# Performance work log

Hardware: AMD Instinct MI355X
Metric: run time of the kernel (lower is better)

## Reference

```python
import jax, jax.numpy as jnp
import numpy as np

N, E, D = 50000, 800000, 128
CLAMP = 2.0  # coord_weights_clamp_value


def setup_inputs() -> dict:
    key = jax.random.key(0)
    ks = jax.random.split(key, 12)
    rn = lambda k, shape, scale: jax.random.normal(k, shape, jnp.float32) * scale
    s = lambda fan_in: 1.0 / np.sqrt(fan_in)
    h = rn(ks[0], (N, D), 1.0)
    x = rn(ks[1], (N, 3), 1.0)
    edges = jax.random.randint(ks[2], (2, E), 0, N)
    # edge MLP: Linear(2D+1 -> D), SiLU, Linear(D -> D), SiLU
    we1 = rn(ks[3], (2 * D + 1, D), s(2 * D + 1)); be1 = jnp.zeros((D,), jnp.float32)
    we2 = rn(ks[4], (D, D), s(D));                 be2 = jnp.zeros((D,), jnp.float32)
    # node MLP: Linear(2D -> D), SiLU, Linear(D -> D)
    wn1 = rn(ks[5], (2 * D, D), s(2 * D));         bn1 = jnp.zeros((D,), jnp.float32)
    wn2 = rn(ks[6], (D, D), s(D));                 bn2 = jnp.zeros((D,), jnp.float32)
    # coord MLP: Linear(D -> D), SiLU, Linear(D -> 1, no bias, small init)
    wc1 = rn(ks[7], (D, D), s(D));                 bc1 = jnp.zeros((D,), jnp.float32)
    wc2 = rn(ks[8], (D, 1), 0.001)
    return dict(h=h, x=x, edges=edges, we1=we1, be1=be1, we2=we2, be2=be2,
                wn1=wn1, bn1=bn1, wn2=wn2, bn2=bn2, wc1=wc1, bc1=bc1, wc2=wc2)


def reference(h, x, edges, we1, be1, we2, be2, wn1, bn1, wn2, bn2, wc1, bc1, wc2):
    n = h.shape[0]
    row, col = edges[0], edges[1]
    # coord2radial
    coord_diff = x[row] - x[col]                                  # [E, 3]
    radial = jnp.sum(coord_diff * coord_diff, axis=1, keepdims=True)  # [E, 1]
    # edge model: phi_e(h_i, h_j, ||x_i - x_j||^2)
    e_in = jnp.concatenate([h[row], h[col], radial], axis=1)      # [E, 2D+1]
    m = jax.nn.silu(jax.nn.silu(e_in @ we1 + be1) @ we2 + be2)    # [E, D]
    # coord model: x_i += mean_j (x_i - x_j) * phi_x(m_ij), clamped
    w = jax.nn.silu(m @ wc1 + bc1) @ wc2                          # [E, 1]
    trans = jnp.clip(coord_diff * w, -CLAMP, CLAMP)               # [E, 3]
    ones = jnp.ones((row.shape[0], 1), m.dtype)
    cnt = jax.ops.segment_sum(ones, row, num_segments=n)          # [N, 1]
    agg_x = jax.ops.segment_sum(trans, row, num_segments=n) / jnp.maximum(cnt, 1.0)
    x_out = x + agg_x
    # node model: h_i += phi_h(h_i, sum_j m_ij)  (residual=True)
    agg_m = jax.ops.segment_sum(m, row, num_segments=n)           # [N, D]
    h_up = jax.nn.silu(jnp.concatenate([h, agg_m], axis=1) @ wn1 + bn1) @ wn2 + bn2
    h_out = h + h_up
    return (h_out, x_out)
```

## Files before the change

### kernel.cpp

```cpp
#include <hip/hip_runtime.h>
#include <hip/hip_bf16.h>
#include <stdint.h>

typedef unsigned short u16;
typedef __bf16 bf16x8 __attribute__((ext_vector_type(8)));
typedef float f32x4 __attribute__((ext_vector_type(4)));
typedef unsigned int u32x4 __attribute__((ext_vector_type(4)));

#define DD 128

__device__ __forceinline__ u16 f2bf(float f) {
  uint32_t r;
  asm("v_cvt_pk_bf16_f32 %0, %1, %2" : "=v"(r) : "v"(f), "v"(f));
  return (u16)r;
}
__device__ __forceinline__ float bf2f(u16 h) {
  union { uint32_t u; float f; } v; v.u = ((uint32_t)h) << 16;
  return v.f;
}
__device__ __forceinline__ uint32_t pack2(float a, float b) {
  uint32_t r;
  asm("v_cvt_pk_bf16_f32 %0, %1, %2" : "=v"(r) : "v"(a), "v"(b));
  return r;
}
__device__ __forceinline__ float silu_(float v) {
  return v * __builtin_amdgcn_rcpf(1.0f + __expf(-v));
}
__device__ __forceinline__ f32x4 MFMA(bf16x8 a, bf16x8 b, f32x4 c) {
  return __builtin_amdgcn_mfma_f32_16x16x32_bf16(a, b, c, 0, 0, 0);
}
#define LGKM_FENCE() do { asm volatile("s_waitcnt lgkmcnt(0)" ::: "memory"); __builtin_amdgcn_sched_barrier(0); } while (0)

__global__ __launch_bounds__(256) void kprep(
    const float* __restrict__ we1, const float* __restrict__ we2,
    const float* __restrict__ wn1, const float* __restrict__ wn2,
    const float* __restrict__ wc1, u16* __restrict__ frags) {
  const int total = 16384 * 5 + 32768;
  for (int idx = blockIdx.x * blockDim.x + threadIdx.x; idx < total;
       idx += gridDim.x * blockDim.x) {
    const float* src; int segbase;
    if (idx < 16384)      { src = we1;          segbase = 0; }
    else if (idx < 32768) { src = we1 + 16384;  segbase = 16384; }
    else if (idx < 49152) { src = we2;          segbase = 32768; }
    else if (idx < 65536) { src = wc1;          segbase = 49152; }
    else if (idx < 81920) { src = wn2;          segbase = 65536; }
    else                  { src = wn1;          segbase = 81920; }
    int local = idx - segbase;
    int k = local >> 7, n = local & 127;
    float v = src[k * 128 + n];
    int s = k >> 5, i = k & 7, g = (k >> 3) & 3;
    int lane = (g << 4) | (n & 15), f = n >> 4;
    frags[segbase + (((s * 8 + f) * 64 + lane) << 3) + i] = f2bf(v);
  }
}

__global__ __launch_bounds__(256) void kradial(
    const int* __restrict__ edges, const float* __restrict__ x,
    uint2* __restrict__ cdr, int E) {
  int i = blockIdx.x * 256 + threadIdx.x;
  if (i >= E) return;
  int r = edges[i], c = edges[E + i];
  float dx = x[r * 3]     - x[c * 3];
  float dy = x[r * 3 + 1] - x[c * 3 + 1];
  float dz = x[r * 3 + 2] - x[c * 3 + 2];
  float rad = dx * dx + dy * dy + dz * dz;
  cdr[i] = make_uint2(pack2(dx, dy), pack2(dz, rad));
}

__global__ __launch_bounds__(256) void kpq(
    const float* __restrict__ h, const float* __restrict__ be1,
    const u16* __restrict__ wA, const u16* __restrict__ wB,
    u16* __restrict__ Pb, u16* __restrict__ Qb, int N) {
  __shared__ u16 act[64 * 128];
  const int tid = threadIdx.x;
  const int w = tid >> 6, l = tid & 63;
  const int lm = l & 15, lh = l >> 4;
  const int base = blockIdx.x * 64;

  {
    const int q = l & 3;
    const int rowL = w * 16 + (l >> 2);
    int node = base + rowL; if (node >= N) node = N - 1;
    const float* hs = h + (size_t)node * 128 + q * 32;
    #pragma unroll
    for (int c4 = 0; c4 < 4; ++c4) {
      float4 v0 = *(const float4*)(hs + c4 * 8);
      float4 v1 = *(const float4*)(hs + c4 * 8 + 4);
      uint4 pk;
      pk.x = pack2(v0.x, v0.y); pk.y = pack2(v0.z, v0.w);
      pk.z = pack2(v1.x, v1.y); pk.w = pack2(v1.z, v1.w);
      int c = q * 4 + c4;
      *(uint4*)&act[rowL * 128 + (((c ^ (rowL & 7))) << 3)] = pk;
    }
  }
  LGKM_FENCE();
  const int rowA = w * 16 + lm, sw = rowA & 7;
  bf16x8 a[4];
  #pragma unroll
  for (int s = 0; s < 4; ++s)
    a[s] = *(const bf16x8*)&act[rowA * 128 + (((4 * s + lh) ^ sw) << 3)];
  float be1r[8];
  #pragma unroll
  for (int f = 0; f < 8; ++f) be1r[f] = be1[16 * f + lm];

  f32x4 acc[8] = {};
  #pragma unroll
  for (int s = 0; s < 4; ++s)
    #pragma unroll
    for (int f = 0; f < 8; ++f)
      acc[f] = MFMA(a[s], *(const bf16x8*)(wA + (((s * 8 + f) * 64 + l) << 3)), acc[f]);
  #pragma unroll
  for (int f = 0; f < 8; ++f)
    #pragma unroll
    for (int r = 0; r < 4; ++r) {
      int row = base + w * 16 + lh * 4 + r;
      Pb[(size_t)row * 128 + 16 * f + lm] = f2bf(acc[f][r] + be1r[f]);
    }

  f32x4 acc2[8] = {};
  #pragma unroll
  for (int s = 0; s < 4; ++s)
    #pragma unroll
    for (int f = 0; f < 8; ++f)
      acc2[f] = MFMA(a[s], *(const bf16x8*)(wB + (((s * 8 + f) * 64 + l) << 3)), acc2[f]);
  #pragma unroll
  for (int f = 0; f < 8; ++f)
    #pragma unroll
    for (int r = 0; r < 4; ++r) {
      int row = base + w * 16 + lh * 4 + r;
      Qb[(size_t)row * 128 + 16 * f + lm] = f2bf(acc2[f][r]);
    }
}

__global__ __launch_bounds__(256) void kedgeP(
    const int* __restrict__ edges, const uint2* __restrict__ cdr,
    const float* __restrict__ we1, const float* __restrict__ be2,
    const float* __restrict__ bc1, const float* __restrict__ wc2,
    const u16* __restrict__ Pb, const u16* __restrict__ Qb,
    const u16* __restrict__ we2f, const u16* __restrict__ wc1f,
    float* __restrict__ aggm, float* __restrict__ aggx, int E) {
  __shared__ u16 act[64 * 128];
  __shared__ float w1c[128];
  const int tid = threadIdx.x;
  if (tid < 128) w1c[tid] = we1[256 * 128 + tid];
  __syncthreads();

  const int w = tid >> 6, l = tid & 63;
  const int lm = l & 15, lh = l >> 4;
  const int el = l >> 2, q = l & 3;
  float be2r[8], bc1r[8], wc2r[8];
  #pragma unroll
  for (int f = 0; f < 8; ++f) {
    be2r[f] = be2[16 * f + lm];
    bc1r[f] = bc1[16 * f + lm];
    wc2r[f] = wc2[16 * f + lm];
  }

  const int tb = blockIdx.x * 256 + w * 64;
  const int rowA = w * 16 + lm, sw = rowA & 7;
  const int rowL = w * 16 + el;

  int rv[4], cv[4]; uint2 cdu[4];
  #pragma unroll
  for (int t = 0; t < 4; ++t) {
    int e = tb + t * 16 + lm;
    int ec = e < E ? e : E - 1;
    rv[t] = edges[ec];
    cv[t] = edges[E + ec];
    cdu[t] = cdr[ec];
  }

  u32x4 Pc[4], Qc[4], Pn[4], Qn[4];
  {
    int rG = __shfl(rv[0], el), cG = __shfl(cv[0], el);
    const u16* Pp = Pb + (size_t)rG * 128 + q * 32;
    const u16* Qp = Qb + (size_t)cG * 128 + q * 32;
    #pragma unroll
    for (int c4 = 0; c4 < 4; ++c4) {
      Pc[c4] = *(const u32x4*)(Pp + c4 * 8);
      Qc[c4] = *(const u32x4*)(Qp + c4 * 8);
    }
  }

  #pragma unroll
  for (int t = 0; t < 4; ++t) {
    {
      float radf = bf2f((u16)(cdu[t].y >> 16));
      float rad = __shfl(radf, el);
      #pragma unroll
      for (int c4 = 0; c4 < 4; ++c4) {
        uint32_t pw[4] = {Pc[c4].x, Pc[c4].y, Pc[c4].z, Pc[c4].w};
        uint32_t qw[4] = {Qc[c4].x, Qc[c4].y, Qc[c4].z, Qc[c4].w};
        uint32_t ow[4];
        #pragma unroll
        for (int jj = 0; jj < 4; ++jj) {
          int fb = q * 32 + c4 * 8 + jj * 2;
          float t0 = bf2f((u16)(pw[jj] & 0xffff)) + bf2f((u16)(qw[jj] & 0xffff)) + rad * w1c[fb];
          float t1 = bf2f((u16)(pw[jj] >> 16))    + bf2f((u16)(qw[jj] >> 16))    + rad * w1c[fb + 1];
          ow[jj] = pack2(silu_(t0), silu_(t1));
        }
        int c = q * 4 + c4;
        *(uint4*)&act[rowL * 128 + ((c ^ (rowL & 7)) << 3)] =
            make_uint4(ow[0], ow[1], ow[2], ow[3]);
      }
    }
    LGKM_FENCE();

    bf16x8 a[4];
    #pragma unroll
    for (int s = 0; s < 4; ++s)
      a[s] = *(const bf16x8*)&act[rowA * 128 + (((4 * s + lh) ^ sw) << 3)];

    if (t < 3) {
      int rG = __shfl(rv[t + 1], el), cG = __shfl(cv[t + 1], el);
      const u16* Pp = Pb + (size_t)rG * 128 + q * 32;
      const u16* Qp = Qb + (size_t)cG * 128 + q * 32;
      #pragma unroll
      for (int c4 = 0; c4 < 4; ++c4) {
        Pn[c4] = *(const u32x4*)(Pp + c4 * 8);
        Qn[c4] = *(const u32x4*)(Qp + c4 * 8);
      }
    }

    f32x4 acc[8] = {};
    #pragma unroll
    for (int s = 0; s < 4; ++s)
      #pragma unroll
      for (int f = 0; f < 8; ++f)
        acc[f] = MFMA(a[s], *(const bf16x8*)(we2f + (((s * 8 + f) * 64 + l) << 3)), acc[f]);

    uint32_t pk_m[8][2];
    #pragma unroll
    for (int f = 0; f < 8; ++f) {
      float mv[4];
      #pragma unroll
      for (int r = 0; r < 4; ++r) {
        mv[r] = silu_(acc[f][r] + be2r[f]);
        int row = w * 16 + lh * 4 + r, col = 16 * f + lm;
        act[row * 128 + (((col >> 3) ^ (row & 7)) << 3) + (col & 7)] = f2bf(mv[r]);
      }
      pk_m[f][0] = pack2(mv[0], mv[1]);
      pk_m[f][1] = pack2(mv[2], mv[3]);
    }
    LGKM_FENCE();

    bf16x8 a2[4];
    #pragma unroll
    for (int s = 0; s < 4; ++s)
      a2[s] = *(const bf16x8*)&act[rowA * 128 + (((4 * s + lh) ^ sw) << 3)];
    f32x4 acc3[8] = {};
    #pragma unroll
    for (int s = 0; s < 4; ++s)
      #pragma unroll
      for (int f = 0; f < 8; ++f)
        acc3[f] = MFMA(a2[s], *(const bf16x8*)(wc1f + (((s * 8 + f) * 64 + l) << 3)), acc3[f]);

    float wp[4] = {0.f, 0.f, 0.f, 0.f};
    #pragma unroll
    for (int f = 0; f < 8; ++f)
      #pragma unroll
      for (int r = 0; r < 4; ++r)
        wp[r] += silu_(acc3[f][r] + bc1r[f]) * wc2r[f];
    #pragma unroll
    for (int r = 0; r < 4; ++r) {
      wp[r] += __shfl_xor(wp[r], 1);
      wp[r] += __shfl_xor(wp[r], 2);
      wp[r] += __shfl_xor(wp[r], 4);
      wp[r] += __shfl_xor(wp[r], 8);
    }

    float cdx = bf2f((u16)(cdu[t].x & 0xffff));
    float cdy = bf2f((u16)(cdu[t].x >> 16));
    float cdz = bf2f((u16)(cdu[t].y & 0xffff));
    int er[4]; bool vr[4];
    float cdxr[4], cdyr[4], cdzr[4];
    #pragma unroll
    for (int r = 0; r < 4; ++r) {
      er[r] = __shfl(rv[t], lh * 4 + r);
      vr[r] = (tb + t * 16 + lh * 4 + r) < E;
      cdxr[r] = __shfl(cdx, lh * 4 + r);
      cdyr[r] = __shfl(cdy, lh * 4 + r);
      cdzr[r] = __shfl(cdz, lh * 4 + r);
    }

    if (lm < 4) {
      #pragma unroll
      for (int r = 0; r < 4; ++r) {
        if (vr[r]) {
          float wv = wp[r];
          float v3;
          if (lm == 0)      v3 = fminf(fmaxf(cdxr[r] * wv, -2.0f), 2.0f);
          else if (lm == 1) v3 = fminf(fmaxf(cdyr[r] * wv, -2.0f), 2.0f);
          else if (lm == 2) v3 = fminf(fmaxf(cdzr[r] * wv, -2.0f), 2.0f);
          else              v3 = 1.0f;
          unsafeAtomicAdd(&aggx[(size_t)er[r] * 4 + lm], v3);
        }
      }
    }

    #pragma unroll
    for (int f = 0; f < 8; ++f)
      #pragma unroll
      for (int r = 0; r < 4; ++r) {
        if (vr[r]) {
          float m = bf2f((u16)((pk_m[f][r >> 1] >> ((r & 1) * 16)) & 0xffff));
          unsafeAtomicAdd(&aggm[(size_t)er[r] * 128 + 16 * f + lm], m);
        }
      }

    if (t < 3) {
      #pragma unroll
      for (int c4 = 0; c4 < 4; ++c4) { Pc[c4] = Pn[c4]; Qc[c4] = Qn[c4]; }
    }
  }
}

__global__ __launch_bounds__(256) void kedge_mono(
    const float* __restrict__ x, const int* __restrict__ edges,
    const float* __restrict__ we1, const float* __restrict__ be2,
    const float* __restrict__ bc1, const float* __restrict__ wc2,
    const u16* __restrict__ Pb, const u16* __restrict__ Qb,
    const u16* __restrict__ we2f, const u16* __restrict__ wc1f,
    float* __restrict__ aggm, float* __restrict__ aggx, int E) {
  __shared__ u16 act[64 * 128];
  __shared__ float w1c[128];
  const int tid = threadIdx.x;
  if (tid < 128) w1c[tid] = we1[256 * 128 + tid];
  __syncthreads();

  const int w = tid >> 6, l = tid & 63;
  const int lm = l & 15, lh = l >> 4;
  float be2r[8], bc1r[8], wc2r[8];
  #pragma unroll
  for (int f = 0; f < 8; ++f) {
    be2r[f] = be2[16 * f + lm];
    bc1r[f] = bc1[16 * f + lm];
    wc2r[f] = wc2[16 * f + lm];
  }

  const int tb = blockIdx.x * 64 + w * 16;
  int eMine = tb + lm;
  int eC = eMine < E ? eMine : E - 1;
  const int rowv = edges[eC];
  const int colv = edges[E + eC];
  float cdx = x[rowv * 3]     - x[colv * 3];
  float cdy = x[rowv * 3 + 1] - x[colv * 3 + 1];
  float cdz = x[rowv * 3 + 2] - x[colv * 3 + 2];
  float radial = cdx * cdx + cdy * cdy + cdz * cdz;

  {
    const int el = l >> 2, q = l & 3;
    int rG = __shfl(rowv, el), cG = __shfl(colv, el);
    float rad = __shfl(radial, el);
    const int rowL = w * 16 + el;
    const u16* Pp = Pb + (size_t)rG * 128 + q * 32;
    const u16* Qp = Qb + (size_t)cG * 128 + q * 32;
    #pragma unroll
    for (int c4 = 0; c4 < 4; ++c4) {
      uint4 pv = *(const uint4*)(Pp + c4 * 8);
      uint4 qv = *(const uint4*)(Qp + c4 * 8);
      uint32_t pw[4] = {pv.x, pv.y, pv.z, pv.w};
      uint32_t qw[4] = {qv.x, qv.y, qv.z, qv.w};
      uint32_t ow[4];
      #pragma unroll
      for (int t2 = 0; t2 < 4; ++t2) {
        int fb = q * 32 + c4 * 8 + t2 * 2;
        float t0 = bf2f((u16)(pw[t2] & 0xffff)) + bf2f((u16)(qw[t2] & 0xffff)) + rad * w1c[fb];
        float t1 = bf2f((u16)(pw[t2] >> 16))    + bf2f((u16)(qw[t2] >> 16))    + rad * w1c[fb + 1];
        ow[t2] = pack2(silu_(t0), silu_(t1));
      }
      int c = q * 4 + c4;
      *(uint4*)&act[rowL * 128 + ((c ^ (rowL & 7)) << 3)] =
          make_uint4(ow[0], ow[1], ow[2], ow[3]);
    }
  }
  LGKM_FENCE();

  const int rowA = w * 16 + lm, sw = rowA & 7;
  bf16x8 a[4];
  #pragma unroll
  for (int s = 0; s < 4; ++s)
    a[s] = *(const bf16x8*)&act[rowA * 128 + (((4 * s + lh) ^ sw) << 3)];

  f32x4 acc[8] = {};
  #pragma unroll
  for (int s = 0; s < 4; ++s)
    #pragma unroll
    for (int f = 0; f < 8; ++f)
      acc[f] = MFMA(a[s], *(const bf16x8*)(we2f + (((s * 8 + f) * 64 + l) << 3)), acc[f]);

  #pragma unroll
  for (int f = 0; f < 8; ++f)
    #pragma unroll
    for (int r = 0; r < 4; ++r) {
      float m = silu_(acc[f][r] + be2r[f]);
      int row = w * 16 + lh * 4 + r, col = 16 * f + lm;
      act[row * 128 + (((col >> 3) ^ (row & 7)) << 3) + (col & 7)] = f2bf(m);
    }
  LGKM_FENCE();

  bf16x8 a2[4];
  #pragma unroll
  for (int s = 0; s < 4; ++s)
    a2[s] = *(const bf16x8*)&act[rowA * 128 + (((4 * s + lh) ^ sw) << 3)];
  f32x4 acc3[8] = {};
  #pragma unroll
  for (int s = 0; s < 4; ++s)
    #pragma unroll
    for (int f = 0; f < 8; ++f)
      acc3[f] = MFMA(a2[s], *(const bf16x8*)(wc1f + (((s * 8 + f) * 64 + l) << 3)), acc3[f]);

  float wp[4] = {0.f, 0.f, 0.f, 0.f};
  #pragma unroll
  for (int f = 0; f < 8; ++f)
    #pragma unroll
    for (int r = 0; r < 4; ++r)
      wp[r] += silu_(acc3[f][r] + bc1r[f]) * wc2r[f];
  #pragma unroll
  for (int r = 0; r < 4; ++r) {
    wp[r] += __shfl_xor(wp[r], 1);
    wp[r] += __shfl_xor(wp[r], 2);
    wp[r] += __shfl_xor(wp[r], 4);
    wp[r] += __shfl_xor(wp[r], 8);
  }
  int er[4]; bool vr[4];
  float cdxr[4], cdyr[4], cdzr[4];
  #pragma unroll
  for (int r = 0; r < 4; ++r) {
    er[r] = __shfl(rowv, lh * 4 + r);
    vr[r] = (tb + lh * 4 + r) < E;
    cdxr[r] = __shfl(cdx, lh * 4 + r);
    cdyr[r] = __shfl(cdy, lh * 4 + r);
    cdzr[r] = __shfl(cdz, lh * 4 + r);
  }

  if (lm < 4) {
    #pragma unroll
    for (int r = 0; r < 4; ++r) {
      if (vr[r]) {
        float wv = wp[r];
        float v3;
        if (lm == 0)      v3 = fminf(fmaxf(cdxr[r] * wv, -2.0f), 2.0f);
        else if (lm == 1) v3 = fminf(fmaxf(cdyr[r] * wv, -2.0f), 2.0f);
        else if (lm == 2) v3 = fminf(fmaxf(cdzr[r] * wv, -2.0f), 2.0f);
        else              v3 = 1.0f;
        unsafeAtomicAdd(&aggx[(size_t)er[r] * 4 + lm], v3);
      }
    }
  }
  #pragma unroll
  for (int f = 0; f < 8; ++f)
    #pragma unroll
    for (int r = 0; r < 4; ++r) {
      if (vr[r]) {
        float m = silu_(acc[f][r] + be2r[f]);
        unsafeAtomicAdd(&aggm[(size_t)er[r] * 128 + 16 * f + lm], m);
      }
    }
}

__global__ __launch_bounds__(256) void knode(
    const float* __restrict__ h, const float* __restrict__ x,
    const float* __restrict__ aggm, const float* __restrict__ aggx,
    const float* __restrict__ bn1, const float* __restrict__ bn2,
    const u16* __restrict__ wn1f, const u16* __restrict__ wn2f,
    float* __restrict__ out, int N) {
  __shared__ u16 act[64 * 256];
  __shared__ u16 act2[64 * 128];
  const int tid = threadIdx.x;
  const int w = tid >> 6, l = tid & 63;
  const int lm = l & 15, lh = l >> 4;
  const int base = blockIdx.x * 64;

  if (tid < 192) {
    int n = base + tid / 3, c = tid - (tid / 3) * 3;
    if (n < N) {
      float ct = fmaxf(aggx[(size_t)n * 4 + 3], 1.0f);
      out[(size_t)N * 128 + (size_t)n * 3 + c] =
          x[(size_t)n * 3 + c] + aggx[(size_t)n * 4 + c] / ct;
    }
  }

  {
    const int q = l & 3;
    const int rowL = w * 16 + (l >> 2);
    int node = base + rowL; if (node >= N) node = N - 1;
    const float* src = (q < 2) ? (h + (size_t)node * 128 + q * 64)
                               : (aggm + (size_t)node * 128 + (q - 2) * 64);
    #pragma unroll
    for (int c8 = 0; c8 < 8; ++c8) {
      float4 v0 = *(const float4*)(src + c8 * 8);
      float4 v1 = *(const float4*)(src + c8 * 8 + 4);
      uint4 pk;
      pk.x = pack2(v0.x, v0.y); pk.y = pack2(v0.z, v0.w);
      pk.z = pack2(v1.x, v1.y); pk.w = pack2(v1.z, v1.w);
      int c = q * 8 + c8;
      *(uint4*)&act[rowL * 256 + ((c ^ (rowL & 7)) << 3)] = pk;
    }
  }
  LGKM_FENCE();

  const int rowA = w * 16 + lm, sw = rowA & 7;
  float bn1r[8], bn2r[8];
  #pragma unroll
  for (int f = 0; f < 8; ++f) {
    bn1r[f] = bn1[16 * f + lm];
    bn2r[f] = bn2[16 * f + lm];
  }
  bf16x8 a[8];
  #pragma unroll
  for (int s = 0; s < 8; ++s)
    a[s] = *(const bf16x8*)&act[rowA * 256 + (((4 * s + lh) ^ sw) << 3)];
  f32x4 acc[8] = {};
  #pragma unroll
  for (int s = 0; s < 8; ++s)
    #pragma unroll
    for (int f = 0; f < 8; ++f)
      acc[f] = MFMA(a[s], *(const bf16x8*)(wn1f + (((s * 8 + f) * 64 + l) << 3)), acc[f]);
  #pragma unroll
  for (int f = 0; f < 8; ++f)
    #pragma unroll
    for (int r = 0; r < 4; ++r) {
      int row = w * 16 + lh * 4 + r, col = 16 * f + lm;
      act2[row * 128 + (((col >> 3) ^ (row & 7)) << 3) + (col & 7)] =
          f2bf(silu_(acc[f][r] + bn1r[f]));
    }
  LGKM_FENCE();

  bf16x8 a2[4];
  #pragma unroll
  for (int s = 0; s < 4; ++s)
    a2[s] = *(const bf16x8*)&act2[rowA * 128 + (((4 * s + lh) ^ sw) << 3)];
  f32x4 acc2[8] = {};
  #pragma unroll
  for (int s = 0; s < 4; ++s)
    #pragma unroll
    for (int f = 0; f < 8; ++f)
      acc2[f] = MFMA(a2[s], *(const bf16x8*)(wn2f + (((s * 8 + f) * 64 + l) << 3)), acc2[f]);
  #pragma unroll
  for (int f = 0; f < 8; ++f)
    #pragma unroll
    for (int r = 0; r < 4; ++r) {
      int n2 = base + w * 16 + lh * 4 + r;
      if (n2 < N) {
        int col = 16 * f + lm;
        out[(size_t)n2 * 128 + col] =
            h[(size_t)n2 * 128 + col] + acc2[f][r] + bn2r[f];
      }
    }
}

extern "C" void kernel_launch(void* const* d_in, const int* in_sizes, int n_in,
                              void* d_out, int out_size, void* d_ws, size_t ws_size,
                              hipStream_t stream) {
  const float* h   = (const float*)d_in[0];
  const float* x   = (const float*)d_in[1];
  const int* edges = (const int*)d_in[2];
  const float* we1 = (const float*)d_in[3];
  const float* be1 = (const float*)d_in[4];
  const float* we2 = (const float*)d_in[5];
  const float* be2 = (const float*)d_in[6];
  const float* wn1 = (const float*)d_in[7];
  const float* bn1 = (const float*)d_in[8];
  const float* wn2 = (const float*)d_in[9];
  const float* bn2 = (const float*)d_in[10];
  const float* wc1 = (const float*)d_in[11];
  const float* bc1 = (const float*)d_in[12];
  const float* wc2 = (const float*)d_in[13];

  const int N = in_sizes[0] / DD;
  const int E = in_sizes[2] / 2;
  const int NT = (N + 63) & ~63;

  u16* Pb    = (u16*)d_ws;
  u16* Qb    = Pb + (size_t)NT * DD;
  u16* frags = Qb + (size_t)NT * DD;
  float* aggm = (float*)(frags + 114688);
  float* aggx = aggm + (size_t)NT * DD;
  uint2* cdr = (uint2*)(aggx + (size_t)NT * 4);

  size_t need_mono = (size_t)NT * DD * 2 * 2 + 114688 * 2 +
                     (size_t)NT * (DD * 4 + 16);
  size_t need_pipe = need_mono + (size_t)E * 8;
  if (ws_size < need_mono) return;

  hipLaunchKernelGGL(kprep, dim3(64), dim3(256), 0, stream,
                     we1, we2, wn1, wn2, wc1, frags);
  hipLaunchKernelGGL(kpq, dim3(NT / 64), dim3(256), 0, stream,
                     h, be1, frags, frags + 16384, Pb, Qb, N);
  hipMemsetAsync(aggm, 0, (size_t)NT * (DD * 4 + 16), stream);

  if (ws_size >= need_pipe) {
    hipLaunchKernelGGL(kradial, dim3((E + 255) / 256), dim3(256), 0, stream,
                       edges, x, cdr, E);
    hipLaunchKernelGGL(kedgeP, dim3((E + 255) / 256), dim3(256), 0, stream,
                       edges, cdr, we1, be2, bc1, wc2, Pb, Qb,
                       frags + 32768, frags + 49152, aggm, aggx, E);
  } else {
    hipLaunchKernelGGL(kedge_mono, dim3((E + 63) / 64), dim3(256), 0, stream,
                       x, edges, we1, be2, bc1, wc2, Pb, Qb,
                       frags + 32768, frags + 49152, aggm, aggx, E);
  }
  hipLaunchKernelGGL(knode, dim3(NT / 64), dim3(256), 0, stream,
                     h, x, aggm, aggx, bn1, bn2,
                     frags + 81920, frags + 65536, (float*)d_out, N);
}
```

Before: 551.1 us.

## Replace pipelined 4-tile edge kernel with one-tile-per-wave slim kernel

The edge kernel now has each wave process a single 16-edge tile instead of looping over four tiles with software-prefetched P/Q gathers. The grid is four times larger. MFMA accumulators are split into two halves of four, and bias loads are done inline instead of kept in registers, all to cut register pressure and raise occupancy. The coordinate atomics are also spread across all 64 lanes rather than 4 lanes per row. The trade-off is losing the explicit gather/compute overlap and re-running the per-block w1c shared-memory setup more often.

```diff
diff --git a/kernel.cpp b/kernel.cpp
--- a/kernel.cpp
+++ b/kernel.cpp
@@ -132,12 +132,13 @@
     }
 }
 
-__global__ __launch_bounds__(256) void kedgeP(
+__global__ __launch_bounds__(256) void kedge_slim(
     const int* __restrict__ edges, const uint2* __restrict__ cdr,
-    const float* __restrict__ we1, const float* __restrict__ be2,
-    const float* __restrict__ bc1, const float* __restrict__ wc2,
+    const float* __restrict__ be2, const float* __restrict__ bc1,
+    const float* __restrict__ wc2,
     const u16* __restrict__ Pb, const u16* __restrict__ Qb,
     const u16* __restrict__ we2f, const u16* __restrict__ wc1f,
+    const float* __restrict__ we1,
     float* __restrict__ aggm, float* __restrict__ aggx, int E) {
   __shared__ u16 act[64 * 128];
   __shared__ float w1c[128];
@@ -148,171 +149,139 @@
   const int w = tid >> 6, l = tid & 63;
   const int lm = l & 15, lh = l >> 4;
   const int el = l >> 2, q = l & 3;
-  float be2r[8], bc1r[8], wc2r[8];
-  #pragma unroll
-  for (int f = 0; f < 8; ++f) {
-    be2r[f] = be2[16 * f + lm];
-    bc1r[f] = bc1[16 * f + lm];
-    wc2r[f] = wc2[16 * f + lm];
-  }
-
-  const int tb = blockIdx.x * 256 + w * 64;
-  const int rowA = w * 16 + lm, sw = rowA & 7;
-  const int rowL = w * 16 + el;
-
-  int rv[4], cv[4]; uint2 cdu[4];
-  #pragma unroll
-  for (int t = 0; t < 4; ++t) {
-    int e = tb + t * 16 + lm;
-    int ec = e < E ? e : E - 1;
-    rv[t] = edges[ec];
-    cv[t] = edges[E + ec];
-    cdu[t] = cdr[ec];
-  }
-
-  u32x4 Pc[4], Qc[4], Pn[4], Qn[4];
+
+  const int tb = blockIdx.x * 64 + w * 16;
+  int eMine = tb + lm;
+  int eC = eMine < E ? eMine : E - 1;
+  const int rowv = edges[eC];
+  const int colv = edges[E + eC];
+  const uint2 cdu = cdr[eC];
+
   {
-    int rG = __shfl(rv[0], el), cG = __shfl(cv[0], el);
+    int rG = __shfl(rowv, el), cG = __shfl(colv, el);
+    float radf = bf2f((u16)(cdu.y >> 16));
+    float rad = __shfl(radf, el);
+    const int rowL = w * 16 + el;
     const u16* Pp = Pb + (size_t)rG * 128 + q * 32;
     const u16* Qp = Qb + (size_t)cG * 128 + q * 32;
     #pragma unroll
     for (int c4 = 0; c4 < 4; ++c4) {
-      Pc[c4] = *(const u32x4*)(Pp + c4 * 8);
-      Qc[c4] = *(const u32x4*)(Qp + c4 * 8);
-    }
-  }
-
-  #pragma unroll
-  for (int t = 0; t < 4; ++t) {
-    {
-      float radf = bf2f((u16)(cdu[t].y >> 16));
-      float rad = __shfl(radf, el);
+      u32x4 pv = *(const u32x4*)(Pp + c4 * 8);
+      u32x4 qv = *(const u32x4*)(Qp + c4 * 8);
+      uint32_t pw[4] = {pv.x, pv.y, pv.z, pv.w};
+      uint32_t qw[4] = {qv.x, qv.y, qv.z, qv.w};
+      uint32_t ow[4];
       #pragma unroll
-      for (int c4 = 0; c4 < 4; ++c4) {
-        uint32_t pw[4] = {Pc[c4].x, Pc[c4].y, Pc[c4].z, Pc[c4].w};
-        uint32_t qw[4] = {Qc[c4].x, Qc[c4].y, Qc[c4].z, Qc[c4].w};
-        uint32_t ow[4];
-        #pragma unroll
-        for (int jj = 0; jj < 4; ++jj) {
-          int fb = q * 32 + c4 * 8 + jj * 2;
-          float t0 = bf2f((u16)(pw[jj] & 0xffff)) + bf2f((u16)(qw[jj] & 0xffff)) + rad * w1c[fb];
-          float t1 = bf2f((u16)(pw[jj] >> 16))    + bf2f((u16)(qw[jj] >> 16))    + rad * w1c[fb + 1];
-          ow[jj] = pack2(silu_(t0), silu_(t1));
-        }
-        int c = q * 4 + c4;
-        *(uint4*)&act[rowL * 128 + ((c ^ (rowL & 7)) << 3)] =
-            make_uint4(ow[0], ow[1], ow[2], ow[3]);
-      }
-    }
-    LGKM_FENCE();
-
-    bf16x8 a[4];
-    #pragma unroll
-    for (int s = 0; s < 4; ++s)
-      a[s] = *(const bf16x8*)&act[rowA * 128 + (((4 * s + lh) ^ sw) << 3)];
-
-    if (t < 3) {
-      int rG = __shfl(rv[t + 1], el), cG = __shfl(cv[t + 1], el);
-      const u16* Pp = Pb + (size_t)rG * 128 + q * 32;
-      const u16* Qp = Qb + (size_t)cG * 128 + q * 32;
-      #pragma unroll
-      for (int c4 = 0; c4 < 4; ++c4) {
-        Pn[c4] = *(const u32x4*)(Pp + c4 * 8);
-        Qn[c4] = *(const u32x4*)(Qp + c4 * 8);
-      }
-    }
-
-    f32x4 acc[8] = {};
+      for (int jj = 0; jj < 4; ++jj) {
+        int fb = q * 32 + c4 * 8 + jj * 2;
+        float t0 = bf2f((u16)(pw[jj] & 0xffff)) + bf2f((u16)(qw[jj] & 0xffff)) + rad * w1c[fb];
+        float t1 = bf2f((u16)(pw[jj] >> 16))    + bf2f((u16)(qw[jj] >> 16))    + rad * w1c[fb + 1];
+        ow[jj] = pack2(silu_(t0), silu_(t1));
+      }
+      int c = q * 4 + c4;
+      *(uint4*)&act[rowL * 128 + ((c ^ (rowL & 7)) << 3)] =
+          make_uint4(ow[0], ow[1], ow[2], ow[3]);
+    }
+  }
+  LGKM_FENCE();
+
+  const int rowA = w * 16 + lm, sw = rowA & 7;
+  bf16x8 a[4];
+  #pragma unroll
+  for (int s = 0; s < 4; ++s)
+    a[s] = *(const bf16x8*)&act[rowA * 128 + (((4 * s + lh) ^ sw) << 3)];
+
+  uint32_t pk_m[8][2];
+  #pragma unroll
+  for (int half = 0; half < 2; ++half) {
+    f32x4 acc[4] = {};
     #pragma unroll
     for (int s = 0; s < 4; ++s)
       #pragma unroll
-      for (int f = 0; f < 8; ++f)
-        acc[f] = MFMA(a[s], *(const bf16x8*)(we2f + (((s * 8 + f) * 64 + l) << 3)), acc[f]);
-
-    uint32_t pk_m[8][2];
-    #pragma unroll
-    for (int f = 0; f < 8; ++f) {
+      for (int f = 0; f < 4; ++f)
+        acc[f] = MFMA(a[s],
+            *(const bf16x8*)(we2f + (((s * 8 + half * 4 + f) * 64 + l) << 3)),
+            acc[f]);
+    #pragma unroll
+    for (int f = 0; f < 4; ++f) {
+      const int F = half * 4 + f;
+      float be2v = be2[16 * F + lm];
       float mv[4];
       #pragma unroll
       for (int r = 0; r < 4; ++r) {
-        mv[r] = silu_(acc[f][r] + be2r[f]);
-        int row = w * 16 + lh * 4 + r, col = 16 * f + lm;
+        mv[r] = silu_(acc[f][r] + be2v);
+        int row = w * 16 + lh * 4 + r, col = 16 * F + lm;
         act[row * 128 + (((col >> 3) ^ (row & 7)) << 3) + (col & 7)] = f2bf(mv[r]);
       }
-      pk_m[f][0] = pack2(mv[0], mv[1]);
-      pk_m[f][1] = pack2(mv[2], mv[3]);
-    }
-    LGKM_FENCE();
-
-    bf16x8 a2[4];
-    #pragma unroll
-    for (int s = 0; s < 4; ++s)
-      a2[s] = *(const bf16x8*)&act[rowA * 128 + (((4 * s + lh) ^ sw) << 3)];
-    f32x4 acc3[8] = {};
+      pk_m[F][0] = pack2(mv[0], mv[1]);
+      pk_m[F][1] = pack2(mv[2], mv[3]);
+    }
+  }
+  LGKM_FENCE();
+
+  bf16x8 a2[4];
+  #pragma unroll
+  for (int s = 0; s < 4; ++s)
+    a2[s] = *(const bf16x8*)&act[rowA * 128 + (((4 * s + lh) ^ sw) << 3)];
+  float wp[4] = {0.f, 0.f, 0.f, 0.f};
+  #pragma unroll
+  for (int half = 0; half < 2; ++half) {
+    f32x4 acc3[4] = {};
     #pragma unroll
     for (int s = 0; s < 4; ++s)
       #pragma unroll
-      for (int f = 0; f < 8; ++f)
-        acc3[f] = MFMA(a2[s], *(const bf16x8*)(wc1f + (((s * 8 + f) * 64 + l) << 3)), acc3[f]);
-
-    float wp[4] = {0.f, 0.f, 0.f, 0.f};
-    #pragma unroll
-    for (int f = 0; f < 8; ++f)
+      for (int f = 0; f < 4; ++f)
+        acc3[f] = MFMA(a2[s],
+            *(const bf16x8*)(wc1f + (((s * 8 + half * 4 + f) * 64 + l) << 3)),
+            acc3[f]);
+    #pragma unroll
+    for (int f = 0; f < 4; ++f) {
+      const int F = half * 4 + f;
+      float bc1v = bc1[16 * F + lm];
+      float wc2v = wc2[16 * F + lm];
       #pragma unroll
       for (int r = 0; r < 4; ++r)
-        wp[r] += silu_(acc3[f][r] + bc1r[f]) * wc2r[f];
-    #pragma unroll
-    for (int r = 0; r < 4; ++r) {
-      wp[r] += __shfl_xor(wp[r], 1);
-      wp[r] += __shfl_xor(wp[r], 2);
-      wp[r] += __shfl_xor(wp[r], 4);
-      wp[r] += __shfl_xor(wp[r], 8);
-    }
-
-    float cdx = bf2f((u16)(cdu[t].x & 0xffff));
-    float cdy = bf2f((u16)(cdu[t].x >> 16));
-    float cdz = bf2f((u16)(cdu[t].y & 0xffff));
-    int er[4]; bool vr[4];
-    float cdxr[4], cdyr[4], cdzr[4];
-    #pragma unroll
-    for (int r = 0; r < 4; ++r) {
-      er[r] = __shfl(rv[t], lh * 4 + r);
-      vr[r] = (tb + t * 16 + lh * 4 + r) < E;
-      cdxr[r] = __shfl(cdx, lh * 4 + r);
-      cdyr[r] = __shfl(cdy, lh * 4 + r);
-      cdzr[r] = __shfl(cdz, lh * 4 + r);
-    }
-
-    if (lm < 4) {
-      #pragma unroll
-      for (int r = 0; r < 4; ++r) {
-        if (vr[r]) {
-          float wv = wp[r];
-          float v3;
-          if (lm == 0)      v3 = fminf(fmaxf(cdxr[r] * wv, -2.0f), 2.0f);
-          else if (lm == 1) v3 = fminf(fmaxf(cdyr[r] * wv, -2.0f), 2.0f);
-          else if (lm == 2) v3 = fminf(fmaxf(cdzr[r] * wv, -2.0f), 2.0f);
-          else              v3 = 1.0f;
-          unsafeAtomicAdd(&aggx[(size_t)er[r] * 4 + lm], v3);
-        }
-      }
-    }
-
-    #pragma unroll
-    for (int f = 0; f < 8; ++f)
-      #pragma unroll
-      for (int r = 0; r < 4; ++r) {
-        if (vr[r]) {
-          float m = bf2f((u16)((pk_m[f][r >> 1] >> ((r & 1) * 16)) & 0xffff));
-          unsafeAtomicAdd(&aggm[(size_t)er[r] * 128 + 16 * f + lm], m);
-        }
-      }
-
-    if (t < 3) {
-      #pragma unroll
-      for (int c4 = 0; c4 < 4; ++c4) { Pc[c4] = Pn[c4]; Qc[c4] = Qn[c4]; }
-    }
-  }
+        wp[r] += silu_(acc3[f][r] + bc1v) * wc2v;
+    }
+  }
+  #pragma unroll
+  for (int r = 0; r < 4; ++r) {
+    wp[r] += __shfl_xor(wp[r], 1);
+    wp[r] += __shfl_xor(wp[r], 2);
+    wp[r] += __shfl_xor(wp[r], 4);
+    wp[r] += __shfl_xor(wp[r], 8);
+  }
+
+  {
+    int k = l >> 2;
+    int comp = l & 3;
+    int rr = k & 3;
+    float wpk = rr == 0 ? wp[0] : rr == 1 ? wp[1] : rr == 2 ? wp[2] : wp[3];
+    float cdxk = __shfl(bf2f((u16)(cdu.x & 0xffff)), k);
+    float cdyk = __shfl(bf2f((u16)(cdu.x >> 16)), k);
+    float cdzk = __shfl(bf2f((u16)(cdu.y & 0xffff)), k);
+    int erk = __shfl(rowv, k);
+    float cdv = comp == 0 ? cdxk : comp == 1 ? cdyk : cdzk;
+    float v3 = comp == 3 ? 1.0f : fminf(fmaxf(cdv * wpk, -2.0f), 2.0f);
+    if (tb + k < E)
+      unsafeAtomicAdd(&aggx[(size_t)erk * 4 + comp], v3);
+  }
+
+  int er[4]; bool vr[4];
+  #pragma unroll
+  for (int r = 0; r < 4; ++r) {
+    er[r] = __shfl(rowv, lh * 4 + r);
+    vr[r] = (tb + lh * 4 + r) < E;
+  }
+  #pragma unroll
+  for (int f = 0; f < 8; ++f)
+    #pragma unroll
+    for (int r = 0; r < 4; ++r) {
+      if (vr[r]) {
+        float m = bf2f((u16)((pk_m[f][r >> 1] >> ((r & 1) * 16)) & 0xffff));
+        unsafeAtomicAdd(&aggm[(size_t)er[r] * 128 + 16 * f + lm], m);
+      }
+    }
 }
 
 __global__ __launch_bounds__(256) void kedge_mono(
@@ -593,9 +562,9 @@
   if (ws_size >= need_pipe) {
     hipLaunchKernelGGL(kradial, dim3((E + 255) / 256), dim3(256), 0, stream,
                        edges, x, cdr, E);
-    hipLaunchKernelGGL(kedgeP, dim3((E + 255) / 256), dim3(256), 0, stream,
-                       edges, cdr, we1, be2, bc1, wc2, Pb, Qb,
-                       frags + 32768, frags + 49152, aggm, aggx, E);
+    hipLaunchKernelGGL(kedge_slim, dim3((E + 63) / 64), dim3(256), 0, stream,
+                       edges, cdr, be2, bc1, wc2, Pb, Qb,
+                       frags + 32768, frags + 49152, we1, aggm, aggx, E);
   } else {
     hipLaunchKernelGGL(kedge_mono, dim3((E + 63) / 64), dim3(256), 0, stream,
                        x, edges, we1, be2, bc1, wc2, Pb, Qb,
```

Result: faster. 473.5 us (-14.1%).
